# Optimization experiments

Measured on AMD Instinct MI355X. Metric: run time of the kernel, lower is better.

The kernel has to match this reference:

```python
import jax, jax.numpy as jnp
import numpy as np

TEMP = 0.1
EPS = 1e-8


def setup_inputs() -> dict:
    key = jax.random.key(0)
    k1, k2, k3, k4 = jax.random.split(key, 4)
    b, c, H, W = 2, 64, 80, 80
    proj_main = jax.random.normal(k1, (b, c, H, W), dtype=jnp.float32)
    proj_ema = jax.random.normal(k2, (b, c, H, W), dtype=jnp.float32)
    label_main = jax.random.randint(k3, (b, H, W), 0, 2, dtype=jnp.int32)
    label_ema = jax.random.randint(k4, (b, H, W), 0, 2, dtype=jnp.int32)
    return {"proj_main": proj_main, "proj_ema": proj_ema,
            "label_main": label_main, "label_ema": label_ema,
            "patch_num": 8}


def reference(proj_main, proj_ema, label_main, label_ema, patch_num):
    # Labels / FC fractions are computed in the original forward but never
    # consumed by ContrastiveLoss, so they do not affect the output.
    # All patches have equal size h*w, so the per-patch-mean-of-means equals
    # the global mean over all b*H*W anchors; negative column ordering is
    # irrelevant to the row-wise logsumexp. Hence the nested loop fuses to:
    b, c, H, W = proj_main.shape
    A = jnp.transpose(proj_main, (0, 2, 3, 1)).reshape(-1, c)  # (N, c) anchors
    E = jnp.transpose(proj_ema, (0, 2, 3, 1)).reshape(-1, c)   # (N, c) ema feats
    pos = jnp.sum(A * E, axis=-1) / TEMP                       # (N,)
    neg = jnp.einsum('nc,mc->nm', A, E) / TEMP                 # (N, N)
    full = jnp.concatenate([pos[:, None], neg], axis=1)        # (N, N+1)
    m = jnp.max(full, axis=1)                                  # (N,) row max
    denom = jnp.sum(jnp.exp(full - m[:, None]), axis=1)        # (N,)
    loss = -jnp.log(jnp.exp(pos - m) / (denom + EPS) + EPS)
    return jnp.mean(loss)
```

## Files before the change

kernel.cpp:

```cpp
#include <hip/hip_runtime.h>
#include <stdint.h>

#define NA 12800
#define CCH 64
#define TB 2048
#define SC 14.4269504088896340736f
#define MARGIN 41.0f
#define FLOOR_LOSS 18.420680743952367f
#define MAXF 6400
#define NPARTS 20
#define SGMAX 8

typedef __attribute__((ext_vector_type(4))) float f32x4;
typedef __attribute__((ext_vector_type(8))) short s16x8;

#if __has_builtin(__builtin_amdgcn_exp2f)
#define EXP2(x) __builtin_amdgcn_exp2f(x)
#else
#define EXP2(x) exp2f(x)
#endif

__device__ __forceinline__ uint16_t f2bf(float x) {
  uint32_t u = __float_as_uint(x);
  return (uint16_t)((u + 0x7FFFu + ((u >> 16) & 1u)) >> 16);
}

__global__ __launch_bounds__(256) void prepscreen_k(const float* __restrict__ pm,
                                                    const float* __restrict__ pe,
                                                    char* __restrict__ A,
                                                    char* __restrict__ E,
                                                    float* __restrict__ P2,
                                                    int* __restrict__ wl,
                                                    int* __restrict__ fidx,
                                                    int* __restrict__ cnt) {
  const int blk = blockIdx.x;
  const int tid = threadIdx.x;
  const int lane = tid & 63;
  const int wid = tid >> 6;
  const int l15 = lane & 15, lhi = lane >> 4;
  const f32x4 z4 = (f32x4){0.f, 0.f, 0.f, 0.f};

  __shared__ float pp[4][64];

  {
    const int n = blk * 64 + lane;
    const int b = n / 6400, p = n - b * 6400;
    const float* am = pm + (size_t)b * CCH * 6400 + p;
    const float* ae = pe + (size_t)b * CCH * 6400 + p;
    char* abase = A + (size_t)(n >> 4) * TB + (n & 15) * 16;
    char* ebase = E + (size_t)(n >> 4) * TB + (n & 15) * 16;

    float pos = 0.0f;
#pragma unroll
    for (int cg2 = 0; cg2 < 2; ++cg2) {
      const int cg = wid * 2 + cg2;
      s16x8 ah, eh;
#pragma unroll
      for (int j = 0; j < 8; ++j) {
        int chn = cg * 8 + j;
        float a = am[(size_t)chn * 6400];
        float e = ae[(size_t)chn * 6400];
        pos = fmaf(a, e, pos);
        ah[j] = (short)f2bf(a * SC);
        eh[j] = (short)f2bf(e);
      }
      const int off = (cg >> 2) * 1024 + (cg & 3) * 256;
      *(s16x8*)(abase + off) = ah;
      *(s16x8*)(ebase + off) = eh;
    }
    pp[wid][lane] = pos;
    __syncthreads();
    if (wid == 0) {
      P2[n] = ((pp[0][lane] + pp[1][lane]) + (pp[2][lane] + pp[3][lane])) * SC;
      fidx[n] = -1;
    }
    __syncthreads();
  }

  {
    s16x8 af[2];
#pragma unroll
    for (int ks = 0; ks < 2; ++ks)
      af[ks] = *(const s16x8*)(A + (size_t)(blk * 4 + wid) * TB + ks * 1024 + lane * 16);

    s16x8 b[8][2];
#pragma unroll
    for (int t = 0; t < 8; ++t) {
      const size_t base_t = (t >= 4) ? ((size_t)CCH * 6400 + (t * 1600 - 6400))
                                     : (size_t)(t * 1600);
#pragma unroll
      for (int kh = 0; kh < 2; ++kh) {
#pragma unroll
        for (int j = 0; j < 8; ++j) {
          int ch = kh * 32 + lhi * 8 + j;
          float e = pe[base_t + (size_t)ch * 6400 + l15];
          b[t][kh][j] = (short)f2bf(e);
        }
      }
    }

    float m4[4];
#pragma unroll
    for (int i = 0; i < 4; ++i) m4[i] = -__builtin_inff();

#pragma unroll
    for (int t = 0; t < 8; ++t) {
      f32x4 a_ = __builtin_amdgcn_mfma_f32_16x16x32_bf16(af[0], b[t][0], z4, 0, 0, 0);
      a_ = __builtin_amdgcn_mfma_f32_16x16x32_bf16(af[1], b[t][1], a_, 0, 0, 0);
#pragma unroll
      for (int j = 0; j < 4; ++j) m4[j] = fmaxf(m4[j], a_[j]);
    }
#pragma unroll
    for (int j = 0; j < 4; ++j) {
      float m = m4[j];
#pragma unroll
      for (int mask = 1; mask < 16; mask <<= 1) m = fmaxf(m, __shfl_xor(m, mask));
      m4[j] = m;
    }
    if (l15 == 0) {
#pragma unroll
      for (int j = 0; j < 4; ++j) {
        int row = blk * 64 + wid * 16 + lhi * 4 + j;
        if (!(m4[j] > P2[row] + MARGIN)) {
          int i = atomicAdd(cnt, 1);
          wl[i] = row;
          fidx[row] = i;
        }
      }
    }
  }
}

__global__ __launch_bounds__(256, 2) void exact_k(const char* __restrict__ A,
                                                  const char* __restrict__ E,
                                                  const int* __restrict__ wl,
                                                  const int* __restrict__ cnt,
                                                  float* __restrict__ Pm,
                                                  float* __restrict__ Ps) {
  const int part = blockIdx.x >> 3;
  const int sg0 = blockIdx.x & 7;
  int nr = *cnt; if (nr > MAXF) nr = MAXF;
  const int tid = threadIdx.x;
  const int lane = tid & 63;
  const int wid = tid >> 6;
  const int wm = wid >> 1, wn = wid & 1;
  const int l15 = lane & 15, lhi = lane >> 4;
  const f32x4 z4 = (f32x4){0.f, 0.f, 0.f, 0.f};

  for (int sg = sg0; sg * 64 < nr; sg += SGMAX) {
    const int sbase = sg * 64 + wm * 32;
    s16x8 af[2][2];
#pragma unroll
    for (int rt = 0; rt < 2; ++rt) {
      int sl = sbase + rt * 16 + l15;
      int n = wl[sl < nr ? sl : 0];
#pragma unroll
      for (int ks = 0; ks < 2; ++ks)
        af[rt][ks] = *(const s16x8*)(A + (size_t)(n >> 4) * TB + ks * 1024 + lhi * 256 + (n & 15) * 16);
    }

    float m8[8], s8[8];
#pragma unroll
    for (int i = 0; i < 8; ++i) { m8[i] = -__builtin_inff(); s8[i] = 0.0f; }

    for (int c = 0; c < 5; ++c) {
      s16x8 b[4][2];
#pragma unroll
      for (int ct = 0; ct < 4; ++ct)
#pragma unroll
        for (int kh = 0; kh < 2; ++kh)
          b[ct][kh] = *(const s16x8*)(E + (size_t)(part * 40 + c * 8 + wn * 4 + ct) * TB + kh * 1024 + lane * 16);

      f32x4 acc[2][4];
#pragma unroll
      for (int ct = 0; ct < 4; ++ct)
#pragma unroll
        for (int rt = 0; rt < 2; ++rt) {
          acc[rt][ct] = __builtin_amdgcn_mfma_f32_16x16x32_bf16(af[rt][0], b[ct][0], z4, 0, 0, 0);
          acc[rt][ct] = __builtin_amdgcn_mfma_f32_16x16x32_bf16(af[rt][1], b[ct][1], acc[rt][ct], 0, 0, 0);
        }

#pragma unroll
      for (int rt = 0; rt < 2; ++rt)
#pragma unroll
        for (int j = 0; j < 4; ++j) {
          const int ri = rt * 4 + j;
          float v0 = acc[rt][0][j], v1 = acc[rt][1][j], v2 = acc[rt][2][j], v3 = acc[rt][3][j];
          float vm = fmaxf(fmaxf(fmaxf(v0, v1), v2), v3);
          float mo = m8[ri];
          float mn = fmaxf(mo, vm);
          float t = (EXP2(v0 - mn) + EXP2(v1 - mn)) + (EXP2(v2 - mn) + EXP2(v3 - mn));
          s8[ri] = fmaf(s8[ri], EXP2(mo - mn), t);
          m8[ri] = mn;
        }
    }

#pragma unroll
    for (int ri = 0; ri < 8; ++ri) {
      float m = m8[ri], s = s8[ri];
#pragma unroll
      for (int mask = 1; mask < 16; mask <<= 1) {
        float mo = __shfl_xor(m, mask);
        float so = __shfl_xor(s, mask);
        float mn = fmaxf(m, mo);
        s = s * EXP2(m - mn) + so * EXP2(mo - mn);
        m = mn;
      }
      m8[ri] = m; s8[ri] = s;
    }
    if (l15 == 0) {
#pragma unroll
      for (int rt = 0; rt < 2; ++rt)
#pragma unroll
        for (int j = 0; j < 4; ++j) {
          int slot = sbase + rt * 16 + lhi * 4 + j;
          if (slot < nr) {
            Pm[(size_t)part * MAXF + slot] = m8[rt * 4 + j];
            Ps[(size_t)part * MAXF + slot] = s8[rt * 4 + j];
          }
        }
    }
  }
}

__global__ __launch_bounds__(256) void final_k(const float* __restrict__ P2,
                                               const int* __restrict__ fidx,
                                               const float* __restrict__ Pm,
                                               const float* __restrict__ Ps,
                                               float* __restrict__ bsum,
                                               int* __restrict__ done,
                                               float* __restrict__ out) {
  int n = blockIdx.x * 256 + threadIdx.x;
  int fi = fidx[n];
  float loss;
  if (fi >= 0 && fi < MAXF) {
    float m = -__builtin_inff(), s = 0.0f;
#pragma unroll
    for (int p = 0; p < NPARTS; ++p) {
      float mi = Pm[(size_t)p * MAXF + fi];
      float si = Ps[(size_t)p * MAXF + fi];
      float mn = fmaxf(m, mi);
      s = s * EXP2(m - mn) + si * EXP2(mi - mn);
      m = mn;
    }
    float p2 = P2[n];
    float mn = fmaxf(m, p2);
    float e = EXP2(p2 - mn);
    float sf = s * EXP2(m - mn) + e;
    loss = -logf(e / (sf + 1e-8f) + 1e-8f);
  } else {
    loss = FLOOR_LOSS;
  }

  __shared__ float red[4];
  __shared__ int lastf;
  float v = loss;
#pragma unroll
  for (int off = 32; off > 0; off >>= 1) v += __shfl_down(v, off);
  if ((threadIdx.x & 63) == 0) red[threadIdx.x >> 6] = v;
  __syncthreads();
  if (threadIdx.x == 0) {
    bsum[blockIdx.x] = (red[0] + red[1]) + (red[2] + red[3]);
    __threadfence();
    lastf = (atomicAdd(done, 1) == (NA / 256) - 1);
  }
  __syncthreads();
  if (lastf && threadIdx.x < 64) {
    __threadfence();
    float t = (threadIdx.x < NA / 256) ? bsum[threadIdx.x] : 0.0f;
#pragma unroll
    for (int off = 32; off > 0; off >>= 1) t += __shfl_down(t, off);
    if (threadIdx.x == 0) out[0] = t * (1.0f / (float)NA);
  }
}

extern "C" void kernel_launch(void* const* d_in, const int* in_sizes, int n_in,
                              void* d_out, int out_size, void* d_ws, size_t ws_size,
                              hipStream_t stream) {
  const float* pm = (const float*)d_in[0];
  const float* pe = (const float*)d_in[1];

  char* ws = (char*)d_ws;
  char* Abuf  = ws;
  char* Ebuf  = ws + 1638400;
  float* P2   = (float*)(ws + 3276800);
  float* Pm   = (float*)(ws + 3328000);
  float* Ps   = (float*)(ws + 3840000);
  int*   wl   = (int*)  (ws + 4352000);
  int*   fidx = (int*)  (ws + 4403200);
  int*   ctr  = (int*)  (ws + 4454400);
  float* bsum = (float*)(ws + 4454528);

  hipMemsetAsync(ctr, 0, 8, stream);
  prepscreen_k<<<NA / 64, 256, 0, stream>>>(pm, pe, Abuf, Ebuf, P2, wl, fidx, ctr);
  exact_k <<<NPARTS * SGMAX, 256, 0, stream>>>(Abuf, Ebuf, wl, ctr, Pm, Ps);
  final_k <<<NA / 256, 256, 0, stream>>>(P2, fidx, Pm, Ps, bsum, ctr + 1, (float*)d_out);
}
```

Before: 33.01 us.

## Replace global atomic worklist with per-block ballot compaction and prefix scans

The screening kernel no longer appends survivor rows through a global atomicAdd. Each block now compacts its own survivors with a wavefront ballot and popcount, and writes a per-block count. The exact and final kernels rebuild global slot offsets with a shared-memory prefix scan, and the exact kernel maps slots to rows by binary search. The final reduction becomes a single 1024-thread block, which drops the memset launch, the atomics and the last-block fence pattern. In exchange it adds a scan to every exact block and serialises the final pass onto one block.

Result: slower. 51.33 us (+55.5%).

```diff
diff --git a/kernel.cpp b/kernel.cpp
--- a/kernel.cpp
+++ b/kernel.cpp
@@ -4,6 +4,7 @@
 #define NA 12800
 #define CCH 64
 #define TB 2048
+#define NSEG 200
 #define SC 14.4269504088896340736f
 #define MARGIN 41.0f
 #define FLOOR_LOSS 18.420680743952367f
@@ -32,7 +33,7 @@
                                                     float* __restrict__ P2,
                                                     int* __restrict__ wl,
                                                     int* __restrict__ fidx,
-                                                    int* __restrict__ cnt) {
+                                                    int* __restrict__ bcnt) {
   const int blk = blockIdx.x;
   const int tid = threadIdx.x;
   const int lane = tid & 63;
@@ -41,6 +42,7 @@
   const f32x4 z4 = (f32x4){0.f, 0.f, 0.f, 0.f};
 
   __shared__ float pp[4][64];
+  __shared__ int flg[64];
 
   {
     const int n = blk * 64 + lane;
@@ -70,10 +72,8 @@
     }
     pp[wid][lane] = pos;
     __syncthreads();
-    if (wid == 0) {
+    if (wid == 0)
       P2[n] = ((pp[0][lane] + pp[1][lane]) + (pp[2][lane] + pp[3][lane])) * SC;
-      fidx[n] = -1;
-    }
     __syncthreads();
   }
 
@@ -120,26 +120,41 @@
     if (l15 == 0) {
 #pragma unroll
       for (int j = 0; j < 4; ++j) {
-        int row = blk * 64 + wid * 16 + lhi * 4 + j;
-        if (!(m4[j] > P2[row] + MARGIN)) {
-          int i = atomicAdd(cnt, 1);
-          wl[i] = row;
-          fidx[row] = i;
-        }
-      }
-    }
-  }
+        int rl = wid * 16 + lhi * 4 + j;
+        flg[rl] = !(m4[j] > P2[blk * 64 + rl] + MARGIN);
+      }
+    }
+  }
+  __syncthreads();
+
+  if (tid < 64) {
+    int f = flg[tid];
+    unsigned long long mask = __ballot(f != 0);
+    int idx = (int)__popcll(mask & ((1ull << lane) - 1));
+    if (f) wl[blk * 64 + idx] = blk * 64 + tid;
+    fidx[blk * 64 + tid] = f ? idx : -1;
+    if (tid == 0) bcnt[blk] = (int)__popcll(mask);
+  }
+}
+
+__device__ __forceinline__ int slot2row(const int* __restrict__ spfx,
+                                        const int* __restrict__ wl, int sl) {
+  int lo = 0, hi = NSEG - 1;
+  while (lo < hi) {
+    int mid = (lo + hi + 1) >> 1;
+    if (spfx[mid] <= sl) lo = mid; else hi = mid - 1;
+  }
+  return wl[lo * 64 + (sl - spfx[lo])];
 }
 
 __global__ __launch_bounds__(256, 2) void exact_k(const char* __restrict__ A,
                                                   const char* __restrict__ E,
                                                   const int* __restrict__ wl,
-                                                  const int* __restrict__ cnt,
+                                                  const int* __restrict__ bcnt,
                                                   float* __restrict__ Pm,
                                                   float* __restrict__ Ps) {
   const int part = blockIdx.x >> 3;
   const int sg0 = blockIdx.x & 7;
-  int nr = *cnt; if (nr > MAXF) nr = MAXF;
   const int tid = threadIdx.x;
   const int lane = tid & 63;
   const int wid = tid >> 6;
@@ -147,13 +162,29 @@
   const int l15 = lane & 15, lhi = lane >> 4;
   const f32x4 z4 = (f32x4){0.f, 0.f, 0.f, 0.f};
 
+  __shared__ int scan[256];
+  __shared__ int spfx[NSEG + 1];
+  scan[tid] = (tid < NSEG) ? bcnt[tid] : 0;
+  __syncthreads();
+#pragma unroll
+  for (int off = 1; off < 256; off <<= 1) {
+    int v = (tid >= off) ? scan[tid - off] : 0;
+    __syncthreads();
+    scan[tid] += v;
+    __syncthreads();
+  }
+  if (tid == 0) spfx[0] = 0;
+  if (tid < NSEG) spfx[tid + 1] = scan[tid];
+  __syncthreads();
+  int nr = spfx[NSEG]; if (nr > MAXF) nr = MAXF;
+
   for (int sg = sg0; sg * 64 < nr; sg += SGMAX) {
     const int sbase = sg * 64 + wm * 32;
     s16x8 af[2][2];
 #pragma unroll
     for (int rt = 0; rt < 2; ++rt) {
       int sl = sbase + rt * 16 + l15;
-      int n = wl[sl < nr ? sl : 0];
+      int n = slot2row(spfx, wl, sl < nr ? sl : 0);
 #pragma unroll
       for (int ks = 0; ks < 2; ++ks)
         af[rt][ks] = *(const s16x8*)(A + (size_t)(n >> 4) * TB + ks * 1024 + lhi * 256 + (n & 15) * 16);
@@ -223,54 +254,93 @@
   }
 }
 
-__global__ __launch_bounds__(256) void final_k(const float* __restrict__ P2,
-                                               const int* __restrict__ fidx,
-                                               const float* __restrict__ Pm,
-                                               const float* __restrict__ Ps,
-                                               float* __restrict__ bsum,
-                                               int* __restrict__ done,
-                                               float* __restrict__ out) {
-  int n = blockIdx.x * 256 + threadIdx.x;
-  int fi = fidx[n];
-  float loss;
-  if (fi >= 0 && fi < MAXF) {
-    float m = -__builtin_inff(), s = 0.0f;
-#pragma unroll
-    for (int p = 0; p < NPARTS; ++p) {
-      float mi = Pm[(size_t)p * MAXF + fi];
-      float si = Ps[(size_t)p * MAXF + fi];
-      float mn = fmaxf(m, mi);
-      s = s * EXP2(m - mn) + si * EXP2(mi - mn);
-      m = mn;
-    }
-    float p2 = P2[n];
-    float mn = fmaxf(m, p2);
-    float e = EXP2(p2 - mn);
-    float sf = s * EXP2(m - mn) + e;
-    loss = -logf(e / (sf + 1e-8f) + 1e-8f);
-  } else {
-    loss = FLOOR_LOSS;
-  }
-
-  __shared__ float red[4];
-  __shared__ int lastf;
-  float v = loss;
+__global__ __launch_bounds__(1024) void final_k(const float* __restrict__ P2,
+                                                const int* __restrict__ fidx,
+                                                const int* __restrict__ bcnt,
+                                                const float* __restrict__ Pm,
+                                                const float* __restrict__ Ps,
+                                                float* __restrict__ out) {
+  const int tid = threadIdx.x;
+  __shared__ int scan[256];
+  __shared__ float rsum[16];
+
+  if (tid < 256) scan[tid] = (tid < NSEG) ? bcnt[tid] : 0;
+  __syncthreads();
+#pragma unroll
+  for (int off = 1; off < 256; off <<= 1) {
+    int v = (tid < 256 && tid >= off) ? scan[tid - off] : 0;
+    __syncthreads();
+    if (tid < 256) scan[tid] += v;
+    __syncthreads();
+  }
+
+  float acc = 0.0f;
+#pragma unroll
+  for (int it = 0; it < NA / 1024; ++it) {
+    int n = it * 1024 + tid;
+    int fl = fidx[n];
+    float loss = FLOOR_LOSS;
+    if (fl >= 0) {
+      int g = n >> 6;
+      int fi = (g ? scan[g - 1] : 0) + fl;
+      if (fi < MAXF) {
+        float m = -__builtin_inff(), s = 0.0f;
+#pragma unroll
+        for (int p = 0; p < NPARTS; ++p) {
+          float mi = Pm[(size_t)p * MAXF + fi];
+          float si = Ps[(size_t)p * MAXF + fi];
+          float mn = fmaxf(m, mi);
+          s = s * EXP2(m - mn) + si * EXP2(mi - mn);
+          m = mn;
+        }
+        float p2 = P2[n];
+        float mn = fmaxf(m, p2);
+        float e = EXP2(p2 - mn);
+        float sf = s * EXP2(m - mn) + e;
+        loss = -logf(e / (sf + 1e-8f) + 1e-8f);
+      }
+    }
+    acc += loss;
+  }
+  {
+    int n = (NA / 1024) * 1024 + tid;
+    if (n < NA) {
+      int fl = fidx[n];
+      float loss = FLOOR_LOSS;
+      if (fl >= 0) {
+        int g = n >> 6;
+        int fi = (g ? scan[g - 1] : 0) + fl;
+        if (fi < MAXF) {
+          float m = -__builtin_inff(), s = 0.0f;
+#pragma unroll
+          for (int p = 0; p < NPARTS; ++p) {
+            float mi = Pm[(size_t)p * MAXF + fi];
+            float si = Ps[(size_t)p * MAXF + fi];
+            float mn = fmaxf(m, mi);
+            s = s * EXP2(m - mn) + si * EXP2(mi - mn);
+            m = mn;
+          }
+          float p2 = P2[n];
+          float mn = fmaxf(m, p2);
+          float e = EXP2(p2 - mn);
+          float sf = s * EXP2(m - mn) + e;
+          loss = -logf(e / (sf + 1e-8f) + 1e-8f);
+        }
+      }
+      acc += loss;
+    }
+  }
+
+  float v = acc;
 #pragma unroll
   for (int off = 32; off > 0; off >>= 1) v += __shfl_down(v, off);
-  if ((threadIdx.x & 63) == 0) red[threadIdx.x >> 6] = v;
-  __syncthreads();
-  if (threadIdx.x == 0) {
-    bsum[blockIdx.x] = (red[0] + red[1]) + (red[2] + red[3]);
-    __threadfence();
-    lastf = (atomicAdd(done, 1) == (NA / 256) - 1);
-  }
-  __syncthreads();
-  if (lastf && threadIdx.x < 64) {
-    __threadfence();
-    float t = (threadIdx.x < NA / 256) ? bsum[threadIdx.x] : 0.0f;
-#pragma unroll
-    for (int off = 32; off > 0; off >>= 1) t += __shfl_down(t, off);
-    if (threadIdx.x == 0) out[0] = t * (1.0f / (float)NA);
+  if ((tid & 63) == 0) rsum[tid >> 6] = v;
+  __syncthreads();
+  if (tid < 64) {
+    float t = (tid < 16) ? rsum[tid] : 0.0f;
+#pragma unroll
+    for (int off = 8; off > 0; off >>= 1) t += __shfl_down(t, off);
+    if (tid == 0) out[0] = t * (1.0f / (float)NA);
   }
 }
 
@@ -288,11 +358,9 @@
   float* Ps   = (float*)(ws + 3840000);
   int*   wl   = (int*)  (ws + 4352000);
   int*   fidx = (int*)  (ws + 4403200);
-  int*   ctr  = (int*)  (ws + 4454400);
-  float* bsum = (float*)(ws + 4454528);
-
-  hipMemsetAsync(ctr, 0, 8, stream);
-  prepscreen_k<<<NA / 64, 256, 0, stream>>>(pm, pe, Abuf, Ebuf, P2, wl, fidx, ctr);
-  exact_k <<<NPARTS * SGMAX, 256, 0, stream>>>(Abuf, Ebuf, wl, ctr, Pm, Ps);
-  final_k <<<NA / 256, 256, 0, stream>>>(P2, fidx, Pm, Ps, bsum, ctr + 1, (float*)d_out);
-}
+  int*   bcnt = (int*)  (ws + 4454400);
+
+  prepscreen_k<<<NA / 64, 256, 0, stream>>>(pm, pe, Abuf, Ebuf, P2, wl, fidx, bcnt);
+  exact_k<<<NPARTS * SGMAX, 256, 0, stream>>>(Abuf, Ebuf, wl, bcnt, Pm, Ps);
+  final_k<<<1, 1024, 0, stream>>>(P2, fidx, bcnt, Pm, Ps, (float*)d_out);
+}
```
